# Kernel tuning notes

Measured on AMD Instinct MI355X. Metric: run time of the kernel, lower is better.

The kernel has to match this reference:

```python
import jax, jax.numpy as jnp
import numpy as np

TEMPERATURE = 0.07
NEG_INF = -1e9  # mask value safe for fp16/bf16 softmax


def setup_inputs() -> dict:
    key = jax.random.key(0)
    features = jax.random.normal(key, (8192, 128), dtype=jnp.float32)
    return {"features": features}


def reference(features):
    # L2-normalize rows
    f = features / jnp.linalg.norm(features, axis=1, keepdims=True)
    n = f.shape[0]          # 2 * batch_size
    b = n // 2
    # [n, n] cosine similarity / temperature
    sim = jnp.matmul(f, f.T) / TEMPERATURE
    idx = jnp.arange(n)
    # positive pair index: i <-> i + b (mod n)
    pos = sim[idx, (idx + b) % n]
    # Per row i, CE with the positive as class 0 over [pos, negatives].
    # Denominator = exp(pos) + sum(negatives) = sum over all j != i,
    # so mask only the diagonal and take a row logsumexp.
    sim_masked = jnp.where(jnp.eye(n, dtype=bool), NEG_INF, sim)
    lse = jax.nn.logsumexp(sim_masked, axis=1)
    return jnp.mean(lse - pos)
```

## Files before the change

### kernel.cpp

```cpp
#include <hip/hip_runtime.h>
#include <hip/hip_bf16.h>
#include <stdint.h>


#define N_ROWS 8192
#define DIM    128
#define HALF_N 4096
#define NBANDS 64
#define BROWS  128
#define NTRI   (NBANDS * (NBANDS + 1) / 2)
#define CHUNK  64
#define NCH    (BROWS / CHUNK)
#define NJT    (CHUNK / 16)

static constexpr float INV_T = 14.285714285714286f;
static constexpr float SCALE = 20.60992915555662f;

typedef __attribute__((ext_vector_type(8))) short short8;
typedef __attribute__((ext_vector_type(4))) float f32x4;

#if __has_builtin(__builtin_amdgcn_exp2f)
__device__ inline float fast_exp2(float x) { return __builtin_amdgcn_exp2f(x); }
#else
__device__ inline float fast_exp2(float x) { return exp2f(x); }
#endif

__device__ inline float bf_lo(uint32_t u) { return __uint_as_float(u << 16); }
__device__ inline float bf_hi(uint32_t u) { return __uint_as_float(u & 0xFFFF0000u); }
__device__ inline uint16_t f2bf(float x) {
    uint32_t u = __float_as_uint(x);
    return (uint16_t)((u + 0x7FFFu + ((u >> 16) & 1u)) >> 16);
}

__device__ inline void load_lds16(const void* g, void* l) {
    __builtin_amdgcn_global_load_lds(
        (const __attribute__((address_space(1))) uint32_t*)g,
        (__attribute__((address_space(3))) uint32_t*)l, 16, 0, 0);
}

__global__ __launch_bounds__(256) void k_normalize(const float* __restrict__ f,
                                                   uint16_t* __restrict__ fn,
                                                   float* __restrict__ E) {
    if (blockIdx.x == 0) {
        float4 z = {0.f, 0.f, 0.f, 0.f};
        #pragma unroll
        for (int i = 0; i < 8; ++i)
            ((float4*)E)[threadIdx.x + i * 256] = z;
    }
    int wid  = (blockIdx.x * blockDim.x + threadIdx.x) >> 6;
    int lane = threadIdx.x & 63;
    const float2* src = (const float2*)(f + (size_t)wid * DIM);
    float2 v = src[lane];
    float ss = v.x * v.x + v.y * v.y;
    #pragma unroll
    for (int m = 1; m < 64; m <<= 1) ss += __shfl_xor(ss, m, 64);
    float inv = rsqrtf(ss);
    ushort2 o;
    o.x = f2bf(v.x * inv);
    o.y = f2bf(v.y * inv);
    ((ushort2*)(fn + (size_t)wid * DIM))[lane] = o;
}

__global__ __launch_bounds__(256) void k_simexp(const uint16_t* __restrict__ fn,
                                                float* __restrict__ E) {
    __shared__ __align__(16) uint16_t Bl[2][CHUNK * DIM];
    int bx = 0, rem = blockIdx.x;
    while (rem >= NBANDS - bx) { rem -= NBANDS - bx; ++bx; }
    const int by = bx + rem;
    const bool diag = (by == bx);

    const int tid  = threadIdx.x;
    const int lane = tid & 63;
    const int w    = tid >> 6;
    const int ib   = bx * BROWS + w * 32;
    const int jb   = by * BROWS;
    const int lr = lane & 15;
    const int lk = lane >> 4;

    const short8* fn8 = (const short8*)fn;

    short8 Af[2][4];
    #pragma unroll
    for (int mt = 0; mt < 2; ++mt)
        #pragma unroll
        for (int kc = 0; kc < 4; ++kc)
            Af[mt][kc] = fn8[(size_t)(ib + mt * 16 + lr) * 16 + kc * 4 + lk];

    float es[2][4];
    #pragma unroll
    for (int mt = 0; mt < 2; ++mt)
        #pragma unroll
        for (int r = 0; r < 4; ++r) es[mt][r] = 0.0f;

    const int scc0 = w * 16 + (lane >> 4);
    #define STAGE(c, buf)                                                     \
        _Pragma("unroll")                                                     \
        for (int i = 0; i < 4; ++i) {                                         \
            int cc = scc0 + i * 4;                                            \
            int lc = (lane & 15) ^ (cc & 7);                                  \
            load_lds16(fn8 + (size_t)(jb + (c) * CHUNK + cc) * 16 + lc,       \
                       &Bl[buf][w * 2048 + i * 512]);                         \
        }

    STAGE(0, 0)

    for (int c = 0; c < NCH; ++c) {
        __syncthreads();
        if (c + 1 < NCH) {
            STAGE(c + 1, (c + 1) & 1)
        }
        const char* bp = (const char*)&Bl[c & 1][0];
        #pragma unroll
        for (int jt = 0; jt < NJT; ++jt) {
            const int rbase = (jt * 16 + lr) * 256;
            short8 Bf[4];
            #pragma unroll
            for (int kc = 0; kc < 4; ++kc)
                Bf[kc] = *(const short8*)(bp + rbase + ((((kc << 2) | lk) ^ (lr & 7)) << 4));
            float cs = 0.0f;
            #pragma unroll
            for (int mt = 0; mt < 2; ++mt) {
                f32x4 acc = {0.0f, 0.0f, 0.0f, 0.0f};
                #pragma unroll
                for (int kc = 0; kc < 4; ++kc)
                    acc = __builtin_amdgcn_mfma_f32_16x16x32_bf16(Af[mt][kc], Bf[kc], acc, 0, 0, 0);
                #pragma unroll
                for (int r = 0; r < 4; ++r) {
                    float e = fast_exp2(fmaf(acc[r], SCALE, -SCALE));
                    es[mt][r] += e;
                    cs += e;
                }
            }
            if (!diag) {
                cs += __shfl_xor(cs, 16, 64);
                cs += __shfl_xor(cs, 32, 64);
                if (lk == 0)
                    atomicAdd(&E[jb + c * CHUNK + jt * 16 + lr], cs);
            }
        }
    }

    #pragma unroll
    for (int mt = 0; mt < 2; ++mt)
        #pragma unroll
        for (int r = 0; r < 4; ++r) {
            float v = es[mt][r];
            v += __shfl_xor(v, 1, 64);
            v += __shfl_xor(v, 2, 64);
            v += __shfl_xor(v, 4, 64);
            v += __shfl_xor(v, 8, 64);
            if (lr == 0)
                atomicAdd(&E[ib + mt * 16 + lk * 4 + r], v);
        }
}

__global__ __launch_bounds__(256) void k_finalize(const uint16_t* __restrict__ fn,
                                                  const float* __restrict__ E,
                                                  float* __restrict__ terms) {
    __shared__ float sm[4];
    int wid  = (blockIdx.x * blockDim.x + threadIdx.x) >> 6;
    int lane = threadIdx.x & 63;
    int partner = (wid + HALF_N) & (N_ROWS - 1);
    const uint32_t* fr = (const uint32_t*)(fn + (size_t)wid * DIM);
    const uint32_t* pr = (const uint32_t*)(fn + (size_t)partner * DIM);
    uint32_t a = fr[lane], p = pr[lane];
    float a0 = bf_lo(a), a1 = bf_hi(a);
    float p0 = bf_lo(p), p1 = bf_hi(p);
    float sd = a0 * a0 + a1 * a1;
    float pd = a0 * p0 + a1 * p1;
    #pragma unroll
    for (int m = 1; m < 64; m <<= 1) {
        sd += __shfl_xor(sd, m, 64);
        pd += __shfl_xor(pd, m, 64);
    }
    if (lane == 0) {
        float ep = E[wid] - fast_exp2(fmaf(sd, SCALE, -SCALE));
        sm[threadIdx.x >> 6] = INV_T + logf(ep) - pd * INV_T;
    }
    __syncthreads();
    if (threadIdx.x == 0)
        terms[blockIdx.x] = sm[0] + sm[1] + sm[2] + sm[3];
}

__global__ __launch_bounds__(256) void k_reduce(const float* __restrict__ terms,
                                                float* __restrict__ out) {
    __shared__ float sm[4];
    float acc = 0.0f;
    for (int i = threadIdx.x; i < N_ROWS / 4; i += 256) acc += terms[i];
    #pragma unroll
    for (int m = 1; m < 64; m <<= 1) acc += __shfl_xor(acc, m, 64);
    if ((threadIdx.x & 63) == 0) sm[threadIdx.x >> 6] = acc;
    __syncthreads();
    if (threadIdx.x == 0)
        out[0] = (sm[0] + sm[1] + sm[2] + sm[3]) * (1.0f / N_ROWS);
}

extern "C" void kernel_launch(void* const* d_in, const int* in_sizes, int n_in,
                              void* d_out, int out_size, void* d_ws, size_t ws_size,
                              hipStream_t stream) {
    const float* feat = (const float*)d_in[0];
    float* out = (float*)d_out;

    uint16_t* fn = (uint16_t*)d_ws;
    float* E     = (float*)((char*)d_ws + (size_t)N_ROWS * DIM * 2);
    float* terms = E + N_ROWS;

    k_normalize<<<dim3(N_ROWS / 4), dim3(256), 0, stream>>>(feat, fn, E);
    k_simexp<<<dim3(NTRI), dim3(256), 0, stream>>>(fn, E);
    k_finalize<<<dim3(N_ROWS / 4), dim3(256), 0, stream>>>(fn, E, terms);
    k_reduce<<<dim3(1), dim3(256), 0, stream>>>(terms, out);
}
```

Before: 43.92 us.

## Drop reduce kernel via atomic output, defer column atomics, overlap A loads

Removes the single-block reduce kernel: the output is zeroed in the normalize kernel and each finalize block atomically adds its scaled partial sum. Inside the similarity kernel, the per-tile column-sum atomics move out of the inner loop into a register array that is flushed after all chunks. The A-fragment global loads are issued after the first LDS stage so the two overlap. This saves one launch and takes atomics off the MFMA path, at the cost of more registers and a float-atomic, order-dependent final sum.

```diff
diff --git a/kernel.cpp b/kernel.cpp
--- a/kernel.cpp
+++ b/kernel.cpp
@@ -40,8 +40,10 @@
 
 __global__ __launch_bounds__(256) void k_normalize(const float* __restrict__ f,
                                                    uint16_t* __restrict__ fn,
-                                                   float* __restrict__ E) {
+                                                   float* __restrict__ E,
+                                                   float* __restrict__ out) {
     if (blockIdx.x == 0) {
+        if (threadIdx.x == 0) out[0] = 0.0f;
         float4 z = {0.f, 0.f, 0.f, 0.f};
         #pragma unroll
         for (int i = 0; i < 8; ++i)
@@ -78,19 +80,6 @@
     const int lk = lane >> 4;
 
     const short8* fn8 = (const short8*)fn;
-
-    short8 Af[2][4];
-    #pragma unroll
-    for (int mt = 0; mt < 2; ++mt)
-        #pragma unroll
-        for (int kc = 0; kc < 4; ++kc)
-            Af[mt][kc] = fn8[(size_t)(ib + mt * 16 + lr) * 16 + kc * 4 + lk];
-
-    float es[2][4];
-    #pragma unroll
-    for (int mt = 0; mt < 2; ++mt)
-        #pragma unroll
-        for (int r = 0; r < 4; ++r) es[mt][r] = 0.0f;
 
     const int scc0 = w * 16 + (lane >> 4);
     #define STAGE(c, buf)                                                     \
@@ -104,6 +93,25 @@
 
     STAGE(0, 0)
 
+    short8 Af[2][4];
+    #pragma unroll
+    for (int mt = 0; mt < 2; ++mt)
+        #pragma unroll
+        for (int kc = 0; kc < 4; ++kc)
+            Af[mt][kc] = fn8[(size_t)(ib + mt * 16 + lr) * 16 + kc * 4 + lk];
+
+    float es[2][4];
+    #pragma unroll
+    for (int mt = 0; mt < 2; ++mt)
+        #pragma unroll
+        for (int r = 0; r < 4; ++r) es[mt][r] = 0.0f;
+    float cs_acc[NCH][NJT];
+    #pragma unroll
+    for (int c = 0; c < NCH; ++c)
+        #pragma unroll
+        for (int jt = 0; jt < NJT; ++jt) cs_acc[c][jt] = 0.0f;
+
+    #pragma unroll
     for (int c = 0; c < NCH; ++c) {
         __syncthreads();
         if (c + 1 < NCH) {
@@ -131,15 +139,22 @@
                     cs += e;
                 }
             }
-            if (!diag) {
+            cs_acc[c][jt] += cs;
+        }
+    }
+
+    if (!diag) {
+        #pragma unroll
+        for (int c = 0; c < NCH; ++c)
+            #pragma unroll
+            for (int jt = 0; jt < NJT; ++jt) {
+                float cs = cs_acc[c][jt];
                 cs += __shfl_xor(cs, 16, 64);
                 cs += __shfl_xor(cs, 32, 64);
                 if (lk == 0)
                     atomicAdd(&E[jb + c * CHUNK + jt * 16 + lr], cs);
             }
-        }
-    }
-
+    }
     #pragma unroll
     for (int mt = 0; mt < 2; ++mt)
         #pragma unroll
@@ -156,7 +171,7 @@
 
 __global__ __launch_bounds__(256) void k_finalize(const uint16_t* __restrict__ fn,
                                                   const float* __restrict__ E,
-                                                  float* __restrict__ terms) {
+                                                  float* __restrict__ out) {
     __shared__ float sm[4];
     int wid  = (blockIdx.x * blockDim.x + threadIdx.x) >> 6;
     int lane = threadIdx.x & 63;
@@ -179,20 +194,7 @@
     }
     __syncthreads();
     if (threadIdx.x == 0)
-        terms[blockIdx.x] = sm[0] + sm[1] + sm[2] + sm[3];
-}
-
-__global__ __launch_bounds__(256) void k_reduce(const float* __restrict__ terms,
-                                                float* __restrict__ out) {
-    __shared__ float sm[4];
-    float acc = 0.0f;
-    for (int i = threadIdx.x; i < N_ROWS / 4; i += 256) acc += terms[i];
-    #pragma unroll
-    for (int m = 1; m < 64; m <<= 1) acc += __shfl_xor(acc, m, 64);
-    if ((threadIdx.x & 63) == 0) sm[threadIdx.x >> 6] = acc;
-    __syncthreads();
-    if (threadIdx.x == 0)
-        out[0] = (sm[0] + sm[1] + sm[2] + sm[3]) * (1.0f / N_ROWS);
+        atomicAdd(out, (sm[0] + sm[1] + sm[2] + sm[3]) * (1.0f / N_ROWS));
 }
 
 extern "C" void kernel_launch(void* const* d_in, const int* in_sizes, int n_in,
@@ -203,10 +205,8 @@
 
     uint16_t* fn = (uint16_t*)d_ws;
     float* E     = (float*)((char*)d_ws + (size_t)N_ROWS * DIM * 2);
-    float* terms = E + N_ROWS;
-
-    k_normalize<<<dim3(N_ROWS / 4), dim3(256), 0, stream>>>(feat, fn, E);
+
+    k_normalize<<<dim3(N_ROWS / 4), dim3(256), 0, stream>>>(feat, fn, E, out);
     k_simexp<<<dim3(NTRI), dim3(256), 0, stream>>>(fn, E);
-    k_finalize<<<dim3(N_ROWS / 4), dim3(256), 0, stream>>>(fn, E, terms);
-    k_reduce<<<dim3(1), dim3(256), 0, stream>>>(terms, out);
-}
+    k_finalize<<<dim3(N_ROWS / 4), dim3(256), 0, stream>>>(fn, E, out);
+}
```

Measured after the change: 64.00 us. 45.7% more time.

## Pre-swizzle normalized features into MFMA fragment layout and drop LDS staging

Applied to the files above, without the earlier changes.

The normalize kernel now also writes a second copy of the bf16 features, laid out so each 16-row tile's MFMA operand fragments are contiguous per lane. The sim/exp kernel then loads A and B fragments straight from global memory with coalesced 16-byte loads. This removes the double-buffered LDS staging, its barriers and the swizzle arithmetic. Column-sum atomics are deferred to the end of the block instead of being issued per tile. The cost is an extra 2 MB write in normalize, more register use for the cached column sums, and reliance on L2/cache hits where B tiles were previously shared through LDS across the four waves.

```diff
diff --git a/kernel.cpp b/kernel.cpp
--- a/kernel.cpp
+++ b/kernel.cpp
@@ -9,9 +9,7 @@
 #define NBANDS 64
 #define BROWS  128
 #define NTRI   (NBANDS * (NBANDS + 1) / 2)
-#define CHUNK  64
-#define NCH    (BROWS / CHUNK)
-#define NJT    (CHUNK / 16)
+#define NJT    (BROWS / 16)
 
 static constexpr float INV_T = 14.285714285714286f;
 static constexpr float SCALE = 20.60992915555662f;
@@ -32,14 +30,10 @@
     return (uint16_t)((u + 0x7FFFu + ((u >> 16) & 1u)) >> 16);
 }
 
-__device__ inline void load_lds16(const void* g, void* l) {
-    __builtin_amdgcn_global_load_lds(
-        (const __attribute__((address_space(1))) uint32_t*)g,
-        (__attribute__((address_space(3))) uint32_t*)l, 16, 0, 0);
-}
 
 __global__ __launch_bounds__(256) void k_normalize(const float* __restrict__ f,
                                                    uint16_t* __restrict__ fn,
+                                                   uint16_t* __restrict__ fnB,
                                                    float* __restrict__ E) {
     if (blockIdx.x == 0) {
         float4 z = {0.f, 0.f, 0.f, 0.f};
@@ -59,85 +53,67 @@
     o.x = f2bf(v.x * inv);
     o.y = f2bf(v.y * inv);
     ((ushort2*)(fn + (size_t)wid * DIM))[lane] = o;
+    int k0 = lane * 2;
+    size_t chunk = (size_t)(wid >> 4) * 256 + (k0 >> 5) * 64 +
+                   ((k0 >> 3) & 3) * 16 + (wid & 15);
+    *(ushort2*)((char*)fnB + chunk * 16 + (k0 & 7) * 2) = o;
 }
 
-__global__ __launch_bounds__(256) void k_simexp(const uint16_t* __restrict__ fn,
+__global__ __launch_bounds__(256) void k_simexp(const uint16_t* __restrict__ fnB,
                                                 float* __restrict__ E) {
-    __shared__ __align__(16) uint16_t Bl[2][CHUNK * DIM];
     int bx = 0, rem = blockIdx.x;
     while (rem >= NBANDS - bx) { rem -= NBANDS - bx; ++bx; }
     const int by = bx + rem;
     const bool diag = (by == bx);
 
-    const int tid  = threadIdx.x;
-    const int lane = tid & 63;
-    const int w    = tid >> 6;
-    const int ib   = bx * BROWS + w * 32;
-    const int jb   = by * BROWS;
+    const int lane = threadIdx.x & 63;
+    const int w    = threadIdx.x >> 6;
     const int lr = lane & 15;
     const int lk = lane >> 4;
+    const int ib = bx * BROWS + w * 32;
+    const int tileA0 = ib >> 4;
+    const int tileB0 = by * NJT;
 
-    const short8* fn8 = (const short8*)fn;
+    const short8* fnB8 = (const short8*)fnB;
 
     short8 Af[2][4];
     #pragma unroll
     for (int mt = 0; mt < 2; ++mt)
         #pragma unroll
         for (int kc = 0; kc < 4; ++kc)
-            Af[mt][kc] = fn8[(size_t)(ib + mt * 16 + lr) * 16 + kc * 4 + lk];
+            Af[mt][kc] = fnB8[(size_t)(tileA0 + mt) * 256 + kc * 64 + lane];
 
     float es[2][4];
     #pragma unroll
     for (int mt = 0; mt < 2; ++mt)
         #pragma unroll
         for (int r = 0; r < 4; ++r) es[mt][r] = 0.0f;
+    float cs_acc[NJT];
+    #pragma unroll
+    for (int jt = 0; jt < NJT; ++jt) cs_acc[jt] = 0.0f;
 
-    const int scc0 = w * 16 + (lane >> 4);
-    #define STAGE(c, buf)                                                     \
-        _Pragma("unroll")                                                     \
-        for (int i = 0; i < 4; ++i) {                                         \
-            int cc = scc0 + i * 4;                                            \
-            int lc = (lane & 15) ^ (cc & 7);                                  \
-            load_lds16(fn8 + (size_t)(jb + (c) * CHUNK + cc) * 16 + lc,       \
-                       &Bl[buf][w * 2048 + i * 512]);                         \
-        }
-
-    STAGE(0, 0)
-
-    for (int c = 0; c < NCH; ++c) {
-        __syncthreads();
-        if (c + 1 < NCH) {
-            STAGE(c + 1, (c + 1) & 1)
-        }
-        const char* bp = (const char*)&Bl[c & 1][0];
+    #pragma unroll
+    for (int jt = 0; jt < NJT; ++jt) {
+        const short8* bp = fnB8 + (size_t)(tileB0 + jt) * 256 + lane;
+        short8 Bf[4];
         #pragma unroll
-        for (int jt = 0; jt < NJT; ++jt) {
-            const int rbase = (jt * 16 + lr) * 256;
-            short8 Bf[4];
+        for (int kc = 0; kc < 4; ++kc)
+            Bf[kc] = bp[kc * 64];
+        float cs = 0.0f;
+        #pragma unroll
+        for (int mt = 0; mt < 2; ++mt) {
+            f32x4 acc = {0.0f, 0.0f, 0.0f, 0.0f};
             #pragma unroll
             for (int kc = 0; kc < 4; ++kc)
-                Bf[kc] = *(const short8*)(bp + rbase + ((((kc << 2) | lk) ^ (lr & 7)) << 4));
-            float cs = 0.0f;
+                acc = __builtin_amdgcn_mfma_f32_16x16x32_bf16(Af[mt][kc], Bf[kc], acc, 0, 0, 0);
             #pragma unroll
-            for (int mt = 0; mt < 2; ++mt) {
-                f32x4 acc = {0.0f, 0.0f, 0.0f, 0.0f};
-                #pragma unroll
-                for (int kc = 0; kc < 4; ++kc)
-                    acc = __builtin_amdgcn_mfma_f32_16x16x32_bf16(Af[mt][kc], Bf[kc], acc, 0, 0, 0);
-                #pragma unroll
-                for (int r = 0; r < 4; ++r) {
-                    float e = fast_exp2(fmaf(acc[r], SCALE, -SCALE));
-                    es[mt][r] += e;
-                    cs += e;
-                }
-            }
-            if (!diag) {
-                cs += __shfl_xor(cs, 16, 64);
-                cs += __shfl_xor(cs, 32, 64);
-                if (lk == 0)
-                    atomicAdd(&E[jb + c * CHUNK + jt * 16 + lr], cs);
+            for (int r = 0; r < 4; ++r) {
+                float e = fast_exp2(fmaf(acc[r], SCALE, -SCALE));
+                es[mt][r] += e;
+                cs += e;
             }
         }
+        cs_acc[jt] = cs;
     }
 
     #pragma unroll
@@ -152,6 +128,16 @@
             if (lr == 0)
                 atomicAdd(&E[ib + mt * 16 + lk * 4 + r], v);
         }
+    if (!diag) {
+        #pragma unroll
+        for (int jt = 0; jt < NJT; ++jt) {
+            float cs = cs_acc[jt];
+            cs += __shfl_xor(cs, 16, 64);
+            cs += __shfl_xor(cs, 32, 64);
+            if (lk == 0)
+                atomicAdd(&E[by * BROWS + jt * 16 + lr], cs);
+        }
+    }
 }
 
 __global__ __launch_bounds__(256) void k_finalize(const uint16_t* __restrict__ fn,
@@ -201,12 +187,13 @@
     const float* feat = (const float*)d_in[0];
     float* out = (float*)d_out;
 
-    uint16_t* fn = (uint16_t*)d_ws;
-    float* E     = (float*)((char*)d_ws + (size_t)N_ROWS * DIM * 2);
-    float* terms = E + N_ROWS;
+    uint16_t* fn  = (uint16_t*)d_ws;
+    uint16_t* fnB = fn + (size_t)N_ROWS * DIM;
+    float* E      = (float*)(fnB + (size_t)N_ROWS * DIM);
+    float* terms  = E + N_ROWS;
 
-    k_normalize<<<dim3(N_ROWS / 4), dim3(256), 0, stream>>>(feat, fn, E);
-    k_simexp<<<dim3(NTRI), dim3(256), 0, stream>>>(fn, E);
+    k_normalize<<<dim3(N_ROWS / 4), dim3(256), 0, stream>>>(feat, fn, fnB, E);
+    k_simexp<<<dim3(NTRI), dim3(256), 0, stream>>>(fnB, E);
     k_finalize<<<dim3(N_ROWS / 4), dim3(256), 0, stream>>>(fn, E, terms);
     k_reduce<<<dim3(1), dim3(256), 0, stream>>>(terms, out);
 }
```

Result: no change. 44.10 us (+0.4%).
